# Kernel optimization log

Measured on AMD Instinct MI355X. Metric: run time of the kernel, lower is better.

Reference implementation:

```python
import jax, jax.numpy as jnp
import numpy as np

B, T, S, H, V = 2, 512, 400, 1024, 50257


def setup_inputs() -> dict:
    key = jax.random.key(0)
    ks = jax.random.split(key, 5)
    x = jax.random.normal(ks[0], (B, T, H), dtype=jnp.float32)
    attn_dist = jax.random.normal(ks[1], (B, T, S), dtype=jnp.float32)
    enc_batch_extend_vocab = jax.random.randint(ks[2], (B, S), 0, V)
    # learned params of nn.Linear(H, V) and nn.Linear(H, 1)
    proj_w = jax.random.normal(ks[3], (V, H), dtype=jnp.float32) * 0.02
    proj_b = jnp.zeros((V,), dtype=jnp.float32)
    pgen_w = jax.random.normal(ks[4], (1, H), dtype=jnp.float32) * 0.02
    pgen_b = jnp.zeros((1,), dtype=jnp.float32)
    return {
        "x": x,
        "attn_dist": attn_dist,
        "enc_batch_extend_vocab": enc_batch_extend_vocab,
        "temp": 1,
        "proj_w": proj_w,
        "proj_b": proj_b,
        "pgen_w": pgen_w,
        "pgen_b": pgen_b,
    }


def reference(x, attn_dist, enc_batch_extend_vocab, temp, proj_w, proj_b, pgen_w, pgen_b):
    # p_gen gate: sigmoid(Linear(H -> 1))  -> [B, T, 1]
    p_gen = jax.nn.sigmoid(jnp.einsum("bth,oh->bto", x, pgen_w) + pgen_b)
    # vocab projection: [B, T, V]
    logit = jnp.einsum("bth,vh->btv", x, proj_w) + proj_b
    vocab_dist = jax.nn.softmax(logit / temp, axis=2)
    vocab_dist_ = p_gen * vocab_dist  # [B, T, V]
    # copy distribution over source tokens: [B, T, S]
    attn = jax.nn.softmax(attn_dist / temp, axis=-1)
    attn_ = (1.0 - p_gen) * attn
    # scatter_add along vocab dim; source ids broadcast over decode steps
    idx = jnp.broadcast_to(enc_batch_extend_vocab[:, None, :], attn_.shape)  # [B, T, S]
    scat = jax.vmap(jax.vmap(lambda vd, ix, a: vd.at[ix].add(a)))
    out = scat(vocab_dist_, idx, attn_)
    return jnp.log(out + 1e-40)
```

## Files before the change

kernel.cpp:

```cpp
#include <hip/hip_runtime.h>
#include <hip/hip_bf16.h>

#define BB 2
#define TT 512
#define SS 400
#define HH 1024
#define VV 50257
#define MM (BB*TT)

#define NTILE 393
#define NT_PAD 400
#define VPAD 50304

typedef __attribute__((ext_vector_type(8))) short short8;
typedef __attribute__((ext_vector_type(4))) float f32x4;

#define AS1 __attribute__((address_space(1)))
#define AS3 __attribute__((address_space(3)))

#define SBAR()  do { asm volatile("s_barrier" ::: "memory"); \
                     __builtin_amdgcn_sched_barrier(0); } while (0)
#define WAITV(n) do { asm volatile("s_waitcnt vmcnt(" #n ")" ::: "memory"); \
                      __builtin_amdgcn_sched_barrier(0); } while (0)
#define WAITL0() do { asm volatile("s_waitcnt lgkmcnt(0)" ::: "memory"); \
                      __builtin_amdgcn_sched_barrier(0); } while (0)

static __device__ __forceinline__ void gl_lds16(const unsigned short* g, unsigned short* l) {
    __builtin_amdgcn_global_load_lds((const AS1 unsigned int*)(g), (AS3 unsigned int*)(l), 16, 0, 0);
}

static __device__ __forceinline__ unsigned short f2bf(float f) {
    union { float f; unsigned u; } x;
    x.f = f;
    unsigned r = x.u + 0x7FFFu + ((x.u >> 16) & 1u);
    return (unsigned short)(r >> 16);
}

static __device__ __forceinline__ float bf2f(unsigned short u) {
    union { unsigned u; float f; } x;
    x.u = ((unsigned)u) << 16;
    return x.f;
}

static __device__ __forceinline__ float get_invtemp(const int* tp) {
    int iv = *tp;
    float f;
    if (iv > 0 && iv < 100000) f = (float)iv;
    else                       f = __int_as_float(iv);
    return 1.0f / f;
}

__global__ void zero1_k(int* a, int na) {
    int i = blockIdx.x * blockDim.x + threadIdx.x;
    int st = gridDim.x * blockDim.x;
    for (int t = i; t < na; t += st) a[t] = 0;
}

__global__ void cvtx_pgen_k(const float* __restrict__ x, const float* __restrict__ pw,
                            const float* __restrict__ pb, unsigned short* __restrict__ xb,
                            float* __restrict__ pgen) {
    int m = blockIdx.x, tid = threadIdx.x;
    float4 v = ((const float4*)(x + (size_t)m * HH))[tid];
    ushort4 o;
    o.x = f2bf(v.x); o.y = f2bf(v.y); o.z = f2bf(v.z); o.w = f2bf(v.w);
    ((ushort4*)(xb + (size_t)m * HH))[tid] = o;
    float4 w4 = ((const float4*)pw)[tid];
    float s = v.x * w4.x + v.y * w4.y + v.z * w4.z + v.w * w4.w;
    for (int off = 32; off; off >>= 1) s += __shfl_down(s, off);
    __shared__ float red[4];
    if ((tid & 63) == 0) red[tid >> 6] = s;
    __syncthreads();
    if (tid == 0) {
        float t = red[0] + red[1] + red[2] + red[3] + pb[0];
        pgen[m] = 1.0f / (1.0f + __expf(-t));
    }
}

__global__ void cvt_w_k(const float* __restrict__ W, unsigned short* __restrict__ Wb) {
    size_t g = (size_t)blockIdx.x * 256 + threadIdx.x;
    size_t e0 = g * 8;
    int v = (int)(e0 >> 10);
    short8 o;
    if (v < VV) {
        float4 a = *(const float4*)(W + e0);
        float4 b = *(const float4*)(W + e0 + 4);
        o[0] = f2bf(a.x); o[1] = f2bf(a.y); o[2] = f2bf(a.z); o[3] = f2bf(a.w);
        o[4] = f2bf(b.x); o[5] = f2bf(b.y); o[6] = f2bf(b.z); o[7] = f2bf(b.w);
    } else {
        o = (short8){0,0,0,0,0,0,0,0};
    }
    *(short8*)(Wb + e0) = o;
}

__global__ void map_build_k(const int* __restrict__ enc, int* __restrict__ mapv) {
    int t = blockIdx.x * blockDim.x + threadIdx.x;
    if (t >= BB * SS) return;
    int b = t / SS, s = t % SS;
    int id = enc[b * SS + s];
    atomicCAS(&mapv[(size_t)b * VV + id], 0, s + 1);
}

__global__ void attn_k(const float* __restrict__ attn, const int* __restrict__ enc,
                       const int* __restrict__ mapv, const float* __restrict__ pgen,
                       float* __restrict__ Aacc, const int* __restrict__ tempp) {
    int m = blockIdx.x, tid = threadIdx.x;
    int b = m >> 9;
    float invt = get_invtemp(tempp);
    __shared__ float sv[SS];
    __shared__ float ev[SS];
    __shared__ int   slt[SS];
    __shared__ float red[256];
    float loc = -1e30f;
    for (int s = tid; s < SS; s += 256) {
        float v = attn[(size_t)m * SS + s] * invt;
        sv[s] = v;
        loc = fmaxf(loc, v);
    }
    red[tid] = loc; __syncthreads();
    for (int h = 128; h; h >>= 1) { if (tid < h) red[tid] = fmaxf(red[tid], red[tid + h]); __syncthreads(); }
    float mx = red[0]; __syncthreads();
    float ls = 0.f;
    for (int s = tid; s < SS; s += 256) {
        float e = __expf(sv[s] - mx);
        ev[s] = e;
        ls += e;
        slt[s] = mapv[(size_t)b * VV + enc[b * SS + s]] - 1;
    }
    red[tid] = ls; __syncthreads();
    for (int h = 128; h; h >>= 1) { if (tid < h) red[tid] += red[tid + h]; __syncthreads(); }
    float scale = (1.0f - pgen[m]) / red[0];
    for (int s0 = tid; s0 < SS; s0 += 256) {
        float a = 0.f;
        for (int s = 0; s < SS; ++s)
            a += (slt[s] == s0) ? ev[s] : 0.f;
        Aacc[(size_t)m * SS + s0] = a * scale;
    }
}

template<int LOGBF>
__global__ __launch_bounds__(256) void gemm10_k(
    const unsigned short* __restrict__ xb, const unsigned short* __restrict__ Wb,
    const float* __restrict__ bias, float* __restrict__ outf,
    unsigned short* __restrict__ outb,
    float* __restrict__ pmax, float* __restrict__ psum,
    const int* __restrict__ tempp) {
    __shared__ unsigned short As0[128 * 64];
    __shared__ unsigned short Bs0[128 * 64];
    __shared__ unsigned short As1[128 * 64];
    __shared__ unsigned short Bs1[128 * 64];
    __shared__ float red_mx[2][2][64];
    __shared__ float red_sm[2][2][64];

    int wgid = blockIdx.x;
    int xcd = wgid & 7;
    int l = wgid >> 3;
    int nt = xcd * 50 + (l >> 3);
    int mt = l & 7;
    if (nt >= NTILE) return;
    int m0 = mt * 128, n0 = nt * 128;

    int tid = threadIdx.x;
    int lane = tid & 63, w = tid >> 6;
    int wr = w >> 1, wc = w & 1;
    int r15 = lane & 15, kg = lane >> 4;

    size_t aoff[4], boff[4];
    int ldst[4];
#pragma unroll
    for (int i = 0; i < 4; i++) {
        int q = i * 256 + tid;
        int row = q >> 3;
        int jc = (q & 7) ^ (row & 7);
        aoff[i] = (size_t)(m0 + row) * HH + jc * 8;
        boff[i] = (size_t)(n0 + row) * HH + jc * 8;
        ldst[i] = (i * 256 + w * 64) * 8;
    }

    f32x4 acc[4][4];
#pragma unroll
    for (int i = 0; i < 4; i++)
#pragma unroll
        for (int j = 0; j < 4; j++) acc[i][j] = (f32x4){0.f, 0.f, 0.f, 0.f};

#define STAGE(A_, B_, k0_) do { \
    _Pragma("unroll") for (int i_ = 0; i_ < 4; i_++) { \
        gl_lds16(xb + aoff[i_] + (k0_), (A_) + ldst[i_]); \
        gl_lds16(Wb + boff[i_] + (k0_), (B_) + ldst[i_]); \
    } } while (0)
#define LOADFRAG(AF_, BF_, A_, B_) do { \
    _Pragma("unroll") for (int h_ = 0; h_ < 2; h_++) { \
        _Pragma("unroll") for (int mi_ = 0; mi_ < 4; mi_++) { \
            int row_ = wr * 64 + mi_ * 16 + r15; \
            int jc_ = ((h_ << 2) | kg) ^ (row_ & 7); \
            AF_[h_ * 4 + mi_] = *(const short8*)&(A_)[row_ * 64 + jc_ * 8]; \
        } \
        _Pragma("unroll") for (int ni_ = 0; ni_ < 4; ni_++) { \
            int row_ = wc * 64 + ni_ * 16 + r15; \
            int jc_ = ((h_ << 2) | kg) ^ (row_ & 7); \
            BF_[h_ * 4 + ni_] = *(const short8*)&(B_)[row_ * 64 + jc_ * 8]; \
        } \
    } } while (0)
#define MFMA32(AF_, BF_) do { \
    __builtin_amdgcn_s_setprio(1); \
    _Pragma("unroll") for (int h_ = 0; h_ < 2; h_++) \
    _Pragma("unroll") for (int mi_ = 0; mi_ < 4; mi_++) \
    _Pragma("unroll") for (int ni_ = 0; ni_ < 4; ni_++) \
        acc[mi_][ni_] = __builtin_amdgcn_mfma_f32_16x16x32_bf16( \
            AF_[h_ * 4 + mi_], BF_[h_ * 4 + ni_], acc[mi_][ni_], 0, 0, 0); \
    __builtin_amdgcn_s_setprio(0); \
    } while (0)

    STAGE(As0, Bs0, 0);
    STAGE(As1, Bs1, 64);

    short8 af[8], bf[8];
    for (int p = 0; p < 7; ++p) {
        int k4 = p * 128;
        WAITV(8);
        SBAR();
        LOADFRAG(af, bf, As0, Bs0);
        WAITL0();
        SBAR();
        STAGE(As0, Bs0, k4 + 128);
        MFMA32(af, bf);
        WAITV(8);
        SBAR();
        LOADFRAG(af, bf, As1, Bs1);
        WAITL0();
        SBAR();
        STAGE(As1, Bs1, k4 + 192);
        MFMA32(af, bf);
    }
    WAITV(8);
    SBAR();
    LOADFRAG(af, bf, As0, Bs0);
    MFMA32(af, bf);
    WAITV(0);
    SBAR();
    LOADFRAG(af, bf, As1, Bs1);
    MFMA32(af, bf);
#undef STAGE
#undef LOADFRAG
#undef MFMA32

    float invt = get_invtemp(tempp);
    float bv[4]; bool vld[4]; int gn[4];
#pragma unroll
    for (int ni = 0; ni < 4; ni++) {
        gn[ni] = n0 + wc * 64 + ni * 16 + r15;
        vld[ni] = gn[ni] < VV;
        bv[ni] = vld[ni] ? bias[gn[ni]] : 0.f;
    }
#pragma unroll
    for (int mi = 0; mi < 4; mi++) {
#pragma unroll
        for (int j = 0; j < 4; j++) {
            float mx = -1e30f;
#pragma unroll
            for (int ni = 0; ni < 4; ni++)
                if (vld[ni]) mx = fmaxf(mx, (acc[mi][ni][j] + bv[ni]) * invt);
            float sm = 0.f;
#pragma unroll
            for (int ni = 0; ni < 4; ni++)
                if (vld[ni]) sm += __expf((acc[mi][ni][j] + bv[ni]) * invt - mx);
#pragma unroll
            for (int o = 1; o < 16; o <<= 1) {
                float m2 = __shfl_xor(mx, o);
                float s2 = __shfl_xor(sm, o);
                float nm = fmaxf(mx, m2);
                sm = sm * __expf(mx - nm) + s2 * __expf(m2 - nm);
                mx = nm;
            }
            if (r15 == 0) {
                red_mx[wr][wc][mi * 16 + kg * 4 + j] = mx;
                red_sm[wr][wc][mi * 16 + kg * 4 + j] = sm;
            }
        }
    }
#pragma unroll
    for (int ni = 0; ni < 4; ni++) {
        if (vld[ni]) {
#pragma unroll
            for (int mi = 0; mi < 4; mi++) {
                int gmb = m0 + wr * 64 + mi * 16 + (kg << 2);
#pragma unroll
                for (int j = 0; j < 4; j++) {
                    int row = gmb + j;
                    if (LOGBF)
                        outb[(size_t)row * VPAD + (row & 3) + gn[ni]] = f2bf(acc[mi][ni][j] + bv[ni]);
                    else
                        outf[(size_t)row * VV + gn[ni]] = acc[mi][ni][j] + bv[ni];
                }
            }
        }
    }
    __syncthreads();
    if (tid < 128) {
        int r = tid & 63, wr2 = tid >> 6;
        float m1 = red_mx[wr2][0][r], s1 = red_sm[wr2][0][r];
        float m2 = red_mx[wr2][1][r], s2 = red_sm[wr2][1][r];
        float nm = fmaxf(m1, m2);
        float s = s1 * __expf(m1 - nm) + s2 * __expf(m2 - nm);
        int gm = m0 + wr2 * 64 + r;
        pmax[(size_t)gm * NT_PAD + nt] = nm;
        psum[(size_t)gm * NT_PAD + nt] = s;
    }
}

__global__ void lse_wave_k(const float* __restrict__ pmax, const float* __restrict__ psum,
                           float* __restrict__ lse) {
    int gw = (blockIdx.x * blockDim.x + threadIdx.x) >> 6;
    int ln = threadIdx.x & 63;
    if (gw >= MM) return;
    const float* pm = pmax + (size_t)gw * NT_PAD;
    const float* ps = psum + (size_t)gw * NT_PAD;
    float M = -1e30f, S = 0.f;
    for (int t = ln; t < NTILE; t += 64) {
        float m2 = pm[t], s2 = ps[t];
        float nm = fmaxf(M, m2);
        S = S * __expf(M - nm) + s2 * __expf(m2 - nm);
        M = nm;
    }
#pragma unroll
    for (int o = 1; o < 64; o <<= 1) {
        float m2 = __shfl_xor(M, o);
        float s2 = __shfl_xor(S, o);
        float nm = fmaxf(M, m2);
        S = S * __expf(M - nm) + s2 * __expf(m2 - nm);
        M = nm;
    }
    if (ln == 0) lse[gw] = M + __logf(S);
}

__global__ void finalize_bf_k(const unsigned short* __restrict__ logb,
                              float* __restrict__ out, const float* __restrict__ pgen,
                              const float* __restrict__ lse, const int* __restrict__ mapv,
                              const float* __restrict__ Aacc, const int* __restrict__ tempp) {
    int m = blockIdx.y;
    int b = m >> 9;
    float invt = get_invtemp(tempp);
    float pg = pgen[m], L = lse[m];
    int sk = (-m) & 3, pad = m & 3;
    int nchunk = (VV - sk) >> 2;
    const unsigned short* lrow = logb + (size_t)m * VPAD + pad;
    const int* mrow = mapv + (size_t)b * VV;
    const float* arow = Aacc + (size_t)m * SS;
    size_t base = (size_t)m * VV;
    int c = blockIdx.x * 256 + threadIdx.x;
    if (c < nchunk) {
        int v0 = sk + 4 * c;
        ushort4 lb = *(const ushort4*)(lrow + v0);
        unsigned short ls[4] = {lb.x, lb.y, lb.z, lb.w};
        float rs[4];
#pragma unroll
        for (int j = 0; j < 4; j++) {
            float p = pg * __expf(bf2f(ls[j]) * invt - L);
            int jm = mrow[v0 + j];
            if (jm) p += arow[jm - 1];
            rs[j] = __logf(p + 1e-40f);
        }
        float4 o4 = {rs[0], rs[1], rs[2], rs[3]};
        *(float4*)(out + base + sk + 4 * c) = o4;
    }
    if (blockIdx.x == 0 && threadIdx.x == 0) {
        for (int v = 0; v < sk; v++) {
            float p = pg * __expf(bf2f(lrow[v]) * invt - L);
            int jm = mrow[v];
            if (jm) p += arow[jm - 1];
            out[base + v] = __logf(p + 1e-40f);
        }
        for (int v = sk + 4 * nchunk; v < VV; v++) {
            float p = pg * __expf(bf2f(lrow[v]) * invt - L);
            int jm = mrow[v];
            if (jm) p += arow[jm - 1];
            out[base + v] = __logf(p + 1e-40f);
        }
    }
}

__global__ void finalize_k(float* __restrict__ out, const float* __restrict__ pgen,
                           const float* __restrict__ lse, const int* __restrict__ mapv,
                           const float* __restrict__ Aacc, const int* __restrict__ tempp) {
    int m = blockIdx.y;
    int b = m >> 9;
    float invt = get_invtemp(tempp);
    float pg = pgen[m], L = lse[m];
    size_t base = (size_t)m * VV;
    const int* mrow = mapv + (size_t)b * VV;
    const float* arow = Aacc + (size_t)m * SS;
    int sk = (-m) & 3;
    int nchunk = (VV - sk) >> 2;
    int c = blockIdx.x * 256 + threadIdx.x;
    if (c < nchunk) {
        int v0 = sk + 4 * c;
        float4 l4 = *(const float4*)(out + base + v0);
        float xs[4] = {l4.x, l4.y, l4.z, l4.w};
        float rs[4];
#pragma unroll
        for (int j = 0; j < 4; j++) {
            float p = pg * __expf(xs[j] * invt - L);
            int jm = mrow[v0 + j];
            if (jm) p += arow[jm - 1];
            rs[j] = __logf(p + 1e-40f);
        }
        float4 o4 = {rs[0], rs[1], rs[2], rs[3]};
        *(float4*)(out + base + v0) = o4;
    }
    if (blockIdx.x == 0 && threadIdx.x == 0) {
        for (int v = 0; v < sk; v++) {
            float p = pg * __expf(out[base + v] * invt - L);
            int jm = mrow[v];
            if (jm) p += arow[jm - 1];
            out[base + v] = __logf(p + 1e-40f);
        }
        for (int v = sk + 4 * nchunk; v < VV; v++) {
            float p = pg * __expf(out[base + v] * invt - L);
            int jm = mrow[v];
            if (jm) p += arow[jm - 1];
            out[base + v] = __logf(p + 1e-40f);
        }
    }
}

__global__ __launch_bounds__(256) void gemm_old_k(
    const unsigned short* __restrict__ xb, const float* __restrict__ W,
    const float* __restrict__ bias, float* __restrict__ out) {
    __shared__ unsigned short As[128][40];
    __shared__ unsigned short Bs[128][40];
    int bid = blockIdx.x;
    int mt = bid & 7;
    int nt = bid >> 3;
    int m0 = mt * 128, n0 = nt * 128;
    int tid = threadIdx.x;
    int lid = tid & 63, w = tid >> 6;
    int wr = w >> 1, wc = w & 1;
    int row16 = lid & 15, kg = lid >> 4;

    f32x4 acc[4][4];
#pragma unroll
    for (int i = 0; i < 4; i++)
#pragma unroll
        for (int j = 0; j < 4; j++) acc[i][j] = (f32x4){0.f, 0.f, 0.f, 0.f};

    int tr = tid >> 3;
    int tc = (tid & 7) << 2;

    for (int kt = 0; kt < HH / 32; ++kt) {
        int k0 = kt * 32;
        __syncthreads();
#pragma unroll
        for (int i = 0; i < 4; i++) {
            int r = tr + 32 * i;
            ushort4 a4 = *(const ushort4*)&xb[(size_t)(m0 + r) * HH + k0 + tc];
            *(ushort4*)&As[r][tc] = a4;
            int v = n0 + r; v = (v < VV) ? v : (VV - 1);
            float4 w4 = *(const float4*)&W[(size_t)v * HH + k0 + tc];
            ushort4 b4;
            b4.x = f2bf(w4.x); b4.y = f2bf(w4.y); b4.z = f2bf(w4.z); b4.w = f2bf(w4.w);
            *(ushort4*)&Bs[r][tc] = b4;
        }
        __syncthreads();
        short8 af[4], bf[4];
#pragma unroll
        for (int i = 0; i < 4; i++) {
            af[i] = *(const short8*)&As[wr * 64 + i * 16 + row16][kg * 8];
            bf[i] = *(const short8*)&Bs[wc * 64 + i * 16 + row16][kg * 8];
        }
#pragma unroll
        for (int mi = 0; mi < 4; mi++)
#pragma unroll
            for (int ni = 0; ni < 4; ni++)
                acc[mi][ni] = __builtin_amdgcn_mfma_f32_16x16x32_bf16(af[mi], bf[ni], acc[mi][ni], 0, 0, 0);
    }
#pragma unroll
    for (int ni = 0; ni < 4; ni++) {
        int gnv = n0 + wc * 64 + ni * 16 + row16;
        if (gnv < VV) {
            float bvv = bias[gnv];
#pragma unroll
            for (int mi = 0; mi < 4; mi++) {
                int gmb = m0 + wr * 64 + mi * 16 + (kg << 2);
#pragma unroll
                for (int j = 0; j < 4; j++)
                    out[(size_t)(gmb + j) * VV + gnv] = acc[mi][ni][j] + bvv;
            }
        }
    }
}

__global__ void rowreduce_k(const float* __restrict__ out, float* __restrict__ lse,
                            const int* __restrict__ tempp) {
    int m = blockIdx.x, tid = threadIdx.x;
    float invt = get_invtemp(tempp);
    const float* row = out + (size_t)m * VV;
    int sk = (-m) & 3;
    int nchunk = (VV - sk) >> 2;
    float mi = -1e30f, si = 0.f;
    for (int c = tid; c < nchunk; c += 256) {
        float4 x4 = *(const float4*)(row + sk + 4 * c);
        float xs[4] = {x4.x, x4.y, x4.z, x4.w};
#pragma unroll
        for (int j = 0; j < 4; j++) {
            float x = xs[j] * invt;
            float nm = fmaxf(mi, x);
            si = si * __expf(mi - nm) + __expf(x - nm);
            mi = nm;
        }
    }
    if (tid == 0) {
        for (int v = 0; v < sk; v++) {
            float x = row[v] * invt;
            float nm = fmaxf(mi, x);
            si = si * __expf(mi - nm) + __expf(x - nm);
            mi = nm;
        }
        for (int v = sk + 4 * nchunk; v < VV; v++) {
            float x = row[v] * invt;
            float nm = fmaxf(mi, x);
            si = si * __expf(mi - nm) + __expf(x - nm);
            mi = nm;
        }
    }
    __shared__ float sm[256], ss[256];
    sm[tid] = mi; ss[tid] = si; __syncthreads();
    for (int h = 128; h; h >>= 1) {
        if (tid < h) {
            float m2 = sm[tid + h], s2 = ss[tid + h];
            float nm = fmaxf(sm[tid], m2);
            ss[tid] = ss[tid] * __expf(sm[tid] - nm) + s2 * __expf(m2 - nm);
            sm[tid] = nm;
        }
        __syncthreads();
    }
    if (tid == 0) lse[m] = sm[0] + __logf(ss[0]);
}

extern "C" void kernel_launch(void* const* d_in, const int* in_sizes, int n_in,
                              void* d_out, int out_size, void* d_ws, size_t ws_size,
                              hipStream_t stream) {
    const float* x      = (const float*)d_in[0];
    const float* attn   = (const float*)d_in[1];
    const int*   enc    = (const int*)d_in[2];
    const int*   temp   = (const int*)d_in[3];
    const float* proj_w = (const float*)d_in[4];
    const float* proj_b = (const float*)d_in[5];
    const float* pgen_w = (const float*)d_in[6];
    const float* pgen_b = (const float*)d_in[7];
    float* out = (float*)d_out;

    char* ws = (char*)d_ws;
    const size_t WB_BYTES = (size_t)VPAD * HH * 2;

    size_t o_wb   = 0;
    size_t o_xb   = o_wb + WB_BYTES;
    size_t o_pgen = o_xb + 2097152;
    size_t o_lse  = o_pgen + 4096;
    size_t o_map  = o_lse + 4096;
    size_t o_aacc = o_map + 402432;
    size_t o_pmax = o_aacc + (size_t)MM * SS * 4;
    size_t o_psum = o_pmax + (size_t)MM * NT_PAD * 4;
    size_t o_logb = o_psum + (size_t)MM * NT_PAD * 4;
    size_t need_mid = o_logb;
    size_t need_big = o_logb + (size_t)MM * VPAD * 2;

    if (ws_size >= need_mid) {
        unsigned short* wb   = (unsigned short*)(ws + o_wb);
        unsigned short* xb   = (unsigned short*)(ws + o_xb);
        float*          pgen = (float*)(ws + o_pgen);
        float*          lse  = (float*)(ws + o_lse);
        int*            mapv = (int*)(ws + o_map);
        float*          Aacc = (float*)(ws + o_aacc);
        float*          pmax = (float*)(ws + o_pmax);
        float*          psum = (float*)(ws + o_psum);
        unsigned short* logb = (unsigned short*)(ws + o_logb);

        zero1_k<<<256, 256, 0, stream>>>(mapv, BB * VV);
        cvtx_pgen_k<<<MM, 256, 0, stream>>>(x, pgen_w, pgen_b, xb, pgen);
        cvt_w_k<<<(VPAD * HH / 8 + 255) / 256, 256, 0, stream>>>(proj_w, wb);
        map_build_k<<<4, 256, 0, stream>>>(enc, mapv);
        attn_k<<<MM, 256, 0, stream>>>(attn, enc, mapv, pgen, Aacc, temp);
        if (ws_size >= need_big) {
            gemm10_k<1><<<8 * NT_PAD, 256, 0, stream>>>(xb, wb, proj_b, out, logb, pmax, psum, temp);
            lse_wave_k<<<256, 256, 0, stream>>>(pmax, psum, lse);
            finalize_bf_k<<<dim3(50, MM), 256, 0, stream>>>(logb, out, pgen, lse, mapv, Aacc, temp);
        } else {
            gemm10_k<0><<<8 * NT_PAD, 256, 0, stream>>>(xb, wb, proj_b, out, logb, pmax, psum, temp);
            lse_wave_k<<<256, 256, 0, stream>>>(pmax, psum, lse);
            finalize_k<<<dim3(50, MM), 256, 0, stream>>>(out, pgen, lse, mapv, Aacc, temp);
        }
    } else {
        unsigned short* xb   = (unsigned short*)(ws + 0);
        float*          pgen = (float*)(ws + 2097152);
        float*          lse  = (float*)(ws + 2101248);
        int*            mapv = (int*)(ws + 2105344);
        float*          Aacc = (float*)(ws + 2507776);

        zero1_k<<<256, 256, 0, stream>>>(mapv, BB * VV);
        cvtx_pgen_k<<<MM, 256, 0, stream>>>(x, pgen_w, pgen_b, xb, pgen);
        map_build_k<<<4, 256, 0, stream>>>(enc, mapv);
        attn_k<<<MM, 256, 0, stream>>>(attn, enc, mapv, pgen, Aacc, temp);
        gemm_old_k<<<8 * NTILE, 256, 0, stream>>>(xb, proj_w, proj_b, out);
        rowreduce_k<<<MM, 256, 0, stream>>>(out, lse, temp);
        finalize_k<<<dim3(50, MM), 256, 0, stream>>>(out, pgen, lse, mapv, Aacc, temp);
    }
}
```

Baseline: 415.9 us.

## Enlarge GEMM tiles to 256x256 with 512-thread workgroups

The fused vocab-projection GEMM moves from 128x128 tiles with 4 waves to 256x256 tiles with 8 waves. Each wave now computes a 128x64 sub-tile, which raises arithmetic intensity and halves the number of partial softmax max/sum entries per row that lse_wave_k must combine. The softmax reduction scratch now reuses the A-tile LDS buffer, and the padded weight buffer grows to cover 197 N-tiles. The risks are higher register pressure (32 accumulator fragments per wave), 128 KB of LDS per block, and a coarser grid of 788 blocks that may balance less evenly across CUs and leaves more wasted padding in the last N-tile.

Result: slower. 509.2 us (+22.4%).

```diff
diff --git a/kernel.cpp b/kernel.cpp
--- a/kernel.cpp
+++ b/kernel.cpp
@@ -9,8 +9,11 @@
 #define MM (BB*TT)
 
 #define NTILE 393
-#define NT_PAD 400
 #define VPAD 50304
+
+#define NT2 197
+#define NT2_PAD 200
+#define VPAD2 50432
 
 typedef __attribute__((ext_vector_type(8))) short short8;
 typedef __attribute__((ext_vector_type(4))) float f32x4;
@@ -138,61 +141,58 @@
 }
 
 template<int LOGBF>
-__global__ __launch_bounds__(256) void gemm10_k(
+__global__ __launch_bounds__(512, 2) void gemm256_k(
     const unsigned short* __restrict__ xb, const unsigned short* __restrict__ Wb,
     const float* __restrict__ bias, float* __restrict__ outf,
     unsigned short* __restrict__ outb,
     float* __restrict__ pmax, float* __restrict__ psum,
     const int* __restrict__ tempp) {
-    __shared__ unsigned short As0[128 * 64];
-    __shared__ unsigned short Bs0[128 * 64];
-    __shared__ unsigned short As1[128 * 64];
-    __shared__ unsigned short Bs1[128 * 64];
-    __shared__ float red_mx[2][2][64];
-    __shared__ float red_sm[2][2][64];
+    __shared__ unsigned short As0[256 * 64];
+    __shared__ unsigned short Bs0[256 * 64];
+    __shared__ unsigned short As1[256 * 64];
+    __shared__ unsigned short Bs1[256 * 64];
 
     int wgid = blockIdx.x;
     int xcd = wgid & 7;
     int l = wgid >> 3;
-    int nt = xcd * 50 + (l >> 3);
-    int mt = l & 7;
-    if (nt >= NTILE) return;
-    int m0 = mt * 128, n0 = nt * 128;
+    int nt = xcd * 25 + (l >> 2);
+    int mt = l & 3;
+    if (nt >= NT2) return;
+    int m0 = mt * 256, n0 = nt * 256;
 
     int tid = threadIdx.x;
     int lane = tid & 63, w = tid >> 6;
-    int wr = w >> 1, wc = w & 1;
+    int wr = w >> 2, wc = w & 3;
     int r15 = lane & 15, kg = lane >> 4;
 
-    size_t aoff[4], boff[4];
-    int ldst[4];
+    int aoffE[4], boffE[4];
 #pragma unroll
     for (int i = 0; i < 4; i++) {
-        int q = i * 256 + tid;
+        int q = i * 512 + tid;
         int row = q >> 3;
         int jc = (q & 7) ^ (row & 7);
-        aoff[i] = (size_t)(m0 + row) * HH + jc * 8;
-        boff[i] = (size_t)(n0 + row) * HH + jc * 8;
-        ldst[i] = (i * 256 + w * 64) * 8;
-    }
-
-    f32x4 acc[4][4];
-#pragma unroll
-    for (int i = 0; i < 4; i++)
+        aoffE[i] = (m0 + row) * HH + jc * 8;
+        boffE[i] = (n0 + row) * HH + jc * 8;
+    }
+
+    f32x4 acc[8][4];
+#pragma unroll
+    for (int i = 0; i < 8; i++)
 #pragma unroll
         for (int j = 0; j < 4; j++) acc[i][j] = (f32x4){0.f, 0.f, 0.f, 0.f};
 
 #define STAGE(A_, B_, k0_) do { \
     _Pragma("unroll") for (int i_ = 0; i_ < 4; i_++) { \
-        gl_lds16(xb + aoff[i_] + (k0_), (A_) + ldst[i_]); \
-        gl_lds16(Wb + boff[i_] + (k0_), (B_) + ldst[i_]); \
+        int q_ = i_ * 512 + tid; \
+        gl_lds16(xb + aoffE[i_] + (k0_), (A_) + q_ * 8); \
+        gl_lds16(Wb + boffE[i_] + (k0_), (B_) + q_ * 8); \
     } } while (0)
 #define LOADFRAG(AF_, BF_, A_, B_) do { \
     _Pragma("unroll") for (int h_ = 0; h_ < 2; h_++) { \
-        _Pragma("unroll") for (int mi_ = 0; mi_ < 4; mi_++) { \
-            int row_ = wr * 64 + mi_ * 16 + r15; \
+        _Pragma("unroll") for (int mi_ = 0; mi_ < 8; mi_++) { \
+            int row_ = wr * 128 + mi_ * 16 + r15; \
             int jc_ = ((h_ << 2) | kg) ^ (row_ & 7); \
-            AF_[h_ * 4 + mi_] = *(const short8*)&(A_)[row_ * 64 + jc_ * 8]; \
+            AF_[h_ * 8 + mi_] = *(const short8*)&(A_)[row_ * 64 + jc_ * 8]; \
         } \
         _Pragma("unroll") for (int ni_ = 0; ni_ < 4; ni_++) { \
             int row_ = wc * 64 + ni_ * 16 + r15; \
@@ -200,20 +200,20 @@
             BF_[h_ * 4 + ni_] = *(const short8*)&(B_)[row_ * 64 + jc_ * 8]; \
         } \
     } } while (0)
-#define MFMA32(AF_, BF_) do { \
+#define MFMA64(AF_, BF_) do { \
     __builtin_amdgcn_s_setprio(1); \
     _Pragma("unroll") for (int h_ = 0; h_ < 2; h_++) \
-    _Pragma("unroll") for (int mi_ = 0; mi_ < 4; mi_++) \
+    _Pragma("unroll") for (int mi_ = 0; mi_ < 8; mi_++) \
     _Pragma("unroll") for (int ni_ = 0; ni_ < 4; ni_++) \
         acc[mi_][ni_] = __builtin_amdgcn_mfma_f32_16x16x32_bf16( \
-            AF_[h_ * 4 + mi_], BF_[h_ * 4 + ni_], acc[mi_][ni_], 0, 0, 0); \
+            AF_[h_ * 8 + mi_], BF_[h_ * 4 + ni_], acc[mi_][ni_], 0, 0, 0); \
     __builtin_amdgcn_s_setprio(0); \
     } while (0)
 
     STAGE(As0, Bs0, 0);
     STAGE(As1, Bs1, 64);
 
-    short8 af[8], bf[8];
+    short8 af[16], bf[8];
     for (int p = 0; p < 7; ++p) {
         int k4 = p * 128;
         WAITV(8);
@@ -222,27 +222,29 @@
         WAITL0();
         SBAR();
         STAGE(As0, Bs0, k4 + 128);
-        MFMA32(af, bf);
+        MFMA64(af, bf);
         WAITV(8);
         SBAR();
         LOADFRAG(af, bf, As1, Bs1);
         WAITL0();
         SBAR();
         STAGE(As1, Bs1, k4 + 192);
-        MFMA32(af, bf);
+        MFMA64(af, bf);
     }
     WAITV(8);
     SBAR();
     LOADFRAG(af, bf, As0, Bs0);
-    MFMA32(af, bf);
+    MFMA64(af, bf);
     WAITV(0);
     SBAR();
     LOADFRAG(af, bf, As1, Bs1);
-    MFMA32(af, bf);
+    MFMA64(af, bf);
 #undef STAGE
 #undef LOADFRAG
-#undef MFMA32
-
+#undef MFMA64
+
+    __syncthreads();
+    float* redf = (float*)As0;
     float invt = get_invtemp(tempp);
     float bv[4]; bool vld[4]; int gn[4];
 #pragma unroll
@@ -252,7 +254,7 @@
         bv[ni] = vld[ni] ? bias[gn[ni]] : 0.f;
     }
 #pragma unroll
-    for (int mi = 0; mi < 4; mi++) {
+    for (int mi = 0; mi < 8; mi++) {
 #pragma unroll
         for (int j = 0; j < 4; j++) {
             float mx = -1e30f;
@@ -272,8 +274,9 @@
                 mx = nm;
             }
             if (r15 == 0) {
-                red_mx[wr][wc][mi * 16 + kg * 4 + j] = mx;
-                red_sm[wr][wc][mi * 16 + kg * 4 + j] = sm;
+                int r = mi * 16 + kg * 4 + j;
+                redf[w * 128 + r] = mx;
+                redf[1024 + w * 128 + r] = sm;
             }
         }
     }
@@ -281,8 +284,8 @@
     for (int ni = 0; ni < 4; ni++) {
         if (vld[ni]) {
 #pragma unroll
-            for (int mi = 0; mi < 4; mi++) {
-                int gmb = m0 + wr * 64 + mi * 16 + (kg << 2);
+            for (int mi = 0; mi < 8; mi++) {
+                int gmb = m0 + wr * 128 + mi * 16 + (kg << 2);
 #pragma unroll
                 for (int j = 0; j < 4; j++) {
                     int row = gmb + j;
@@ -295,15 +298,20 @@
         }
     }
     __syncthreads();
-    if (tid < 128) {
-        int r = tid & 63, wr2 = tid >> 6;
-        float m1 = red_mx[wr2][0][r], s1 = red_sm[wr2][0][r];
-        float m2 = red_mx[wr2][1][r], s2 = red_sm[wr2][1][r];
-        float nm = fmaxf(m1, m2);
-        float s = s1 * __expf(m1 - nm) + s2 * __expf(m2 - nm);
-        int gm = m0 + wr2 * 64 + r;
-        pmax[(size_t)gm * NT_PAD + nt] = nm;
-        psum[(size_t)gm * NT_PAD + nt] = s;
+    if (tid < 256) {
+        int wr2 = tid >> 7, r = tid & 127;
+        float M = -1e30f, S = 0.f;
+#pragma unroll
+        for (int c = 0; c < 4; c++) {
+            int wi = wr2 * 4 + c;
+            float m2 = redf[wi * 128 + r], s2 = redf[1024 + wi * 128 + r];
+            float nm = fmaxf(M, m2);
+            S = S * __expf(M - nm) + s2 * __expf(m2 - nm);
+            M = nm;
+        }
+        int gm = m0 + wr2 * 128 + r;
+        pmax[(size_t)gm * NT2_PAD + nt] = M;
+        psum[(size_t)gm * NT2_PAD + nt] = S;
     }
 }
 
@@ -312,10 +320,10 @@
     int gw = (blockIdx.x * blockDim.x + threadIdx.x) >> 6;
     int ln = threadIdx.x & 63;
     if (gw >= MM) return;
-    const float* pm = pmax + (size_t)gw * NT_PAD;
-    const float* ps = psum + (size_t)gw * NT_PAD;
+    const float* pm = pmax + (size_t)gw * NT2_PAD;
+    const float* ps = psum + (size_t)gw * NT2_PAD;
     float M = -1e30f, S = 0.f;
-    for (int t = ln; t < NTILE; t += 64) {
+    for (int t = ln; t < NT2; t += 64) {
         float m2 = pm[t], s2 = ps[t];
         float nm = fmaxf(M, m2);
         S = S * __expf(M - nm) + s2 * __expf(m2 - nm);
@@ -549,7 +557,7 @@
     float* out = (float*)d_out;
 
     char* ws = (char*)d_ws;
-    const size_t WB_BYTES = (size_t)VPAD * HH * 2;
+    const size_t WB_BYTES = (size_t)VPAD2 * HH * 2;
 
     size_t o_wb   = 0;
     size_t o_xb   = o_wb + WB_BYTES;
@@ -558,8 +566,8 @@
     size_t o_map  = o_lse + 4096;
     size_t o_aacc = o_map + 402432;
     size_t o_pmax = o_aacc + (size_t)MM * SS * 4;
-    size_t o_psum = o_pmax + (size_t)MM * NT_PAD * 4;
-    size_t o_logb = o_psum + (size_t)MM * NT_PAD * 4;
+    size_t o_psum = o_pmax + (size_t)MM * NT2_PAD * 4;
+    size_t o_logb = o_psum + (size_t)MM * NT2_PAD * 4;
     size_t need_mid = o_logb;
     size_t need_big = o_logb + (size_t)MM * VPAD * 2;
 
@@ -576,15 +584,15 @@
 
         zero1_k<<<256, 256, 0, stream>>>(mapv, BB * VV);
         cvtx_pgen_k<<<MM, 256, 0, stream>>>(x, pgen_w, pgen_b, xb, pgen);
-        cvt_w_k<<<(VPAD * HH / 8 + 255) / 256, 256, 0, stream>>>(proj_w, wb);
+        cvt_w_k<<<(VPAD2 * HH / 8) / 256, 256, 0, stream>>>(proj_w, wb);
         map_build_k<<<4, 256, 0, stream>>>(enc, mapv);
         attn_k<<<MM, 256, 0, stream>>>(attn, enc, mapv, pgen, Aacc, temp);
         if (ws_size >= need_big) {
-            gemm10_k<1><<<8 * NT_PAD, 256, 0, stream>>>(xb, wb, proj_b, out, logb, pmax, psum, temp);
+            gemm256_k<1><<<8 * 100, 512, 0, stream>>>(xb, wb, proj_b, out, logb, pmax, psum, temp);
             lse_wave_k<<<256, 256, 0, stream>>>(pmax, psum, lse);
             finalize_bf_k<<<dim3(50, MM), 256, 0, stream>>>(logb, out, pgen, lse, mapv, Aacc, temp);
         } else {
-            gemm10_k<0><<<8 * NT_PAD, 256, 0, stream>>>(xb, wb, proj_b, out, logb, pmax, psum, temp);
+            gemm256_k<0><<<8 * 100, 512, 0, stream>>>(xb, wb, proj_b, out, logb, pmax, psum, temp);
             lse_wave_k<<<256, 256, 0, stream>>>(pmax, psum, lse);
             finalize_k<<<dim3(50, MM), 256, 0, stream>>>(out, pgen, lse, mapv, Aacc, temp);
         }
```
